# Kernel tuning notes

Hardware: AMD Instinct MI355X
Metric: run time of the kernel (lower is better)

The kernel has to match this reference:

```python
import jax, jax.numpy as jnp
import numpy as np

REG_DIAG = 0.01   # per-position regularizer added inside the loop in the original
REG_EPS = 1e-05   # global regularizer added after the loop


def setup_inputs() -> dict:
    key = jax.random.key(0)
    B, C, HW = 32, 128, 3136
    embedding = jax.random.normal(key, (B, C, HW), dtype=jnp.float32)
    return {"embedding": embedding}


def reference(embedding):
    # embedding: (B, C, HW)
    B, C, HW = embedding.shape
    mean = jnp.mean(embedding, axis=0)                     # (C, HW)
    centered = embedding - mean[None, :, :]                # (B, C, HW)
    # Per-position sample covariance: cov[i] = X_m^T X_m / (B-1), X_m = (B, C) slice at position i.
    cov = jnp.einsum('bci,bdi->icd', centered, centered) / (B - 1)  # (HW, C, C)
    eye = jnp.eye(C, dtype=embedding.dtype)
    cov = cov + (REG_DIAG + REG_EPS) * eye[None, :, :]
    inv_covariance = jnp.linalg.inv(cov)                   # batched inverse, (HW, C, C)
    return (mean, inv_covariance)
```

## Files before the change

### kernel.cpp

```cpp
#include <hip/hip_runtime.h>

#define HW 3136
#define NB 32
#define NC 128
#define XST 132
#define SST 36
#define LAMV 0.01001f
#define SIG(r) (((((r) & 1)) << 4) | ((r) >> 1))

static __device__ __forceinline__ float2 pka0(float2 c, float2 v, float2 a) {
  float2 d;
  asm("v_pk_fma_f32 %0, %1, %2, %3 op_sel:[0,0,0] op_sel_hi:[0,1,1]"
      : "=v"(d) : "v"(c), "v"(v), "v"(a));
  return d;
}
static __device__ __forceinline__ float2 pka1(float2 c, float2 v, float2 a) {
  float2 d;
  asm("v_pk_fma_f32 %0, %1, %2, %3 op_sel:[1,0,0] op_sel_hi:[1,1,1]"
      : "=v"(d) : "v"(c), "v"(v), "v"(a));
  return d;
}
static __device__ __forceinline__ float2 pke(float2 a, float2 b, float2 c) {
  float2 d;
  asm("v_pk_fma_f32 %0, %1, %2, %3"
      : "=v"(d) : "v"(a), "v"(b), "v"(c));
  return d;
}

__global__ __launch_bounds__(512, 8)
void mvg_kernel(const float* __restrict__ emb, float* __restrict__ out) {
  const int bid = blockIdx.x;
  const int pos = (bid & 7) * 392 + (bid >> 3);
  const int t = threadIdx.x;

  __shared__ __align__(16) float XcB[NB * XST];
  __shared__ __align__(16) float WB[NB * XST];
  __shared__ __align__(16) float SB[32 * SST];
  __shared__ __align__(16) float ms[NC];

  #pragma unroll
  for (int m = 0; m < 8; ++m) {
    const int idx = t + 512 * m;
    const int b = idx >> 7;
    const int c = idx & (NC - 1);
    XcB[SIG(b) * XST + c] = emb[(size_t)b * (size_t)(NC * HW) + (size_t)c * HW + pos];
  }
  __syncthreads();

  if (t < NC) {
    float s = 0.f;
    #pragma unroll
    for (int b = 0; b < NB; ++b) s += XcB[b * XST + t];
    const float m = s * (1.0f / NB);
    ms[t] = m;
    out[(size_t)t * HW + pos] = m;
  }
  __syncthreads();

  #pragma unroll
  for (int m = 0; m < 8; ++m) {
    const int idx = t + 512 * m;
    const int b = idx >> 7;
    const int c = idx & (NC - 1);
    XcB[b * XST + c] -= ms[c];
  }
  __syncthreads();

  if (t < 136) {
    const float fs = sqrtf(1089.0f - 8.0f * (float)t);
    const int I = (int)floorf((33.0f - fs) * 0.5f);
    const int J = I + t - (I * (33 - I)) / 2;
    const float* xi0 = &XcB[I * XST];
    const float* xi1 = &XcB[(16 + I) * XST];
    const float* xj0 = &XcB[J * XST];
    const float* xj1 = &XcB[(16 + J) * XST];
    float2 d00 = make_float2(0.f, 0.f), d01 = make_float2(0.f, 0.f);
    float2 d10 = make_float2(0.f, 0.f), d11 = make_float2(0.f, 0.f);
    #pragma unroll 8
    for (int c = 0; c < NC; c += 4) {
      const float4 a0 = *(const float4*)&xi0[c];
      const float4 a1 = *(const float4*)&xi1[c];
      const float4 b0 = *(const float4*)&xj0[c];
      const float4 b1 = *(const float4*)&xj1[c];
      const float2 a0L = make_float2(a0.x, a0.y), a0H = make_float2(a0.z, a0.w);
      const float2 a1L = make_float2(a1.x, a1.y), a1H = make_float2(a1.z, a1.w);
      const float2 b0L = make_float2(b0.x, b0.y), b0H = make_float2(b0.z, b0.w);
      const float2 b1L = make_float2(b1.x, b1.y), b1H = make_float2(b1.z, b1.w);
      d00 = pke(a0L, b0L, d00); d00 = pke(a0H, b0H, d00);
      d01 = pke(a0L, b1L, d01); d01 = pke(a0H, b1H, d01);
      d10 = pke(a1L, b0L, d10); d10 = pke(a1H, b0H, d10);
      d11 = pke(a1L, b1L, d11); d11 = pke(a1H, b1H, d11);
    }
    const float s31 = 1.0f / 31.0f;
    const float dg = (I == J) ? LAMV : 0.f;
    float2 e0, e1;
    e0.x = (d00.x + d00.y) * s31 + dg;
    e0.y = (d01.x + d01.y) * s31;
    e1.x = (d10.x + d10.y) * s31;
    e1.y = (d11.x + d11.y) * s31 + dg;
    *(float2*)&SB[I * SST + 2 * J] = e0;
    *(float2*)&SB[(16 + I) * SST + 2 * J] = e1;
    if (I != J) {
      *(float2*)&SB[J * SST + 2 * I] = make_float2(e0.x, e1.x);
      *(float2*)&SB[(16 + J) * SST + 2 * I] = make_float2(e0.y, e1.y);
    }
  }
  __syncthreads();

  if (t < 64) {
    const int r = t & 31;
    const int hb = (t >> 5) << 4;
    const int rs = SIG(r);
    float m[16];
    #pragma unroll
    for (int j = 0; j < 4; ++j) {
      const float4 v = *(const float4*)&SB[rs * SST + hb + 4 * j];
      m[4 * j] = v.x; m[4 * j + 1] = v.y; m[4 * j + 2] = v.z; m[4 * j + 3] = v.w;
    }

    #define SWEEP_K(K) {                                                    \
      float pc = m[(K) & 15] - ((r == (K)) ? 1.0f : 0.0f);                  \
      const float dm1 = __shfl(pc, (((K) >> 4) << 5) + (K), 64);            \
      const float cr  = __shfl(pc, (((K) >> 4) << 5) + r, 64);              \
      const float g = cr * __builtin_amdgcn_rcpf(dm1 + 1.0f);               \
      float hj[16];                                                         \
      _Pragma("unroll")                                                     \
      for (int j = 0; j < 16; ++j)                                          \
        hj[j] = __shfl(pc, (((K) >> 4) << 5) + hb + j, 64);                 \
      _Pragma("unroll")                                                     \
      for (int j = 0; j < 16; ++j) m[j] = fmaf(-g, hj[j], m[j]);            \
    }

    SWEEP_K(0)  SWEEP_K(1)  SWEEP_K(2)  SWEEP_K(3)
    SWEEP_K(4)  SWEEP_K(5)  SWEEP_K(6)  SWEEP_K(7)
    SWEEP_K(8)  SWEEP_K(9)  SWEEP_K(10) SWEEP_K(11)
    SWEEP_K(12) SWEEP_K(13) SWEEP_K(14) SWEEP_K(15)
    SWEEP_K(16) SWEEP_K(17) SWEEP_K(18) SWEEP_K(19)
    SWEEP_K(20) SWEEP_K(21) SWEEP_K(22) SWEEP_K(23)
    SWEEP_K(24) SWEEP_K(25) SWEEP_K(26) SWEEP_K(27)
    SWEEP_K(28) SWEEP_K(29) SWEEP_K(30) SWEEP_K(31)

    #pragma unroll
    for (int j = 0; j < 16; ++j) {
      const int col = hb + j;
      SB[rs * SST + col] = (col == r) ? (2.0f - m[j]) : (-m[j]);
    }
  }
  __syncthreads();

  if (t < 256) {
    const int s2 = t >> 4;
    const int CA = (t & 15) << 2;
    const int CB = 64 + CA;
    float2 w0[4], w1[4];
    #pragma unroll
    for (int q = 0; q < 4; ++q) {
      w0[q] = make_float2(0.f, 0.f);
      w1[q] = make_float2(0.f, 0.f);
    }
    #pragma unroll 2
    for (int j = 0; j < 32; j += 4) {
      const float4 sv0 = *(const float4*)&SB[s2 * SST + j];
      const float4 sv1 = *(const float4*)&SB[(16 + s2) * SST + j];
      const float2 s0L = make_float2(sv0.x, sv0.y), s0H = make_float2(sv0.z, sv0.w);
      const float2 s1L = make_float2(sv1.x, sv1.y), s1H = make_float2(sv1.z, sv1.w);
      const int jh = j >> 1;
      const float* xr0 = &XcB[jh * XST];
      const float* xr1 = &XcB[(16 + jh) * XST];
      const float* xr2 = &XcB[(jh + 1) * XST];
      const float* xr3 = &XcB[(17 + jh) * XST];
      {
        const float4 a = *(const float4*)&xr0[CA];
        const float4 b = *(const float4*)&xr0[CB];
        w0[0] = pka0(s0L, make_float2(a.x, a.y), w0[0]);
        w0[1] = pka0(s0L, make_float2(a.z, a.w), w0[1]);
        w0[2] = pka0(s0L, make_float2(b.x, b.y), w0[2]);
        w0[3] = pka0(s0L, make_float2(b.z, b.w), w0[3]);
        w1[0] = pka0(s1L, make_float2(a.x, a.y), w1[0]);
        w1[1] = pka0(s1L, make_float2(a.z, a.w), w1[1]);
        w1[2] = pka0(s1L, make_float2(b.x, b.y), w1[2]);
        w1[3] = pka0(s1L, make_float2(b.z, b.w), w1[3]);
      }
      {
        const float4 a = *(const float4*)&xr1[CA];
        const float4 b = *(const float4*)&xr1[CB];
        w0[0] = pka1(s0L, make_float2(a.x, a.y), w0[0]);
        w0[1] = pka1(s0L, make_float2(a.z, a.w), w0[1]);
        w0[2] = pka1(s0L, make_float2(b.x, b.y), w0[2]);
        w0[3] = pka1(s0L, make_float2(b.z, b.w), w0[3]);
        w1[0] = pka1(s1L, make_float2(a.x, a.y), w1[0]);
        w1[1] = pka1(s1L, make_float2(a.z, a.w), w1[1]);
        w1[2] = pka1(s1L, make_float2(b.x, b.y), w1[2]);
        w1[3] = pka1(s1L, make_float2(b.z, b.w), w1[3]);
      }
      {
        const float4 a = *(const float4*)&xr2[CA];
        const float4 b = *(const float4*)&xr2[CB];
        w0[0] = pka0(s0H, make_float2(a.x, a.y), w0[0]);
        w0[1] = pka0(s0H, make_float2(a.z, a.w), w0[1]);
        w0[2] = pka0(s0H, make_float2(b.x, b.y), w0[2]);
        w0[3] = pka0(s0H, make_float2(b.z, b.w), w0[3]);
        w1[0] = pka0(s1H, make_float2(a.x, a.y), w1[0]);
        w1[1] = pka0(s1H, make_float2(a.z, a.w), w1[1]);
        w1[2] = pka0(s1H, make_float2(b.x, b.y), w1[2]);
        w1[3] = pka0(s1H, make_float2(b.z, b.w), w1[3]);
      }
      {
        const float4 a = *(const float4*)&xr3[CA];
        const float4 b = *(const float4*)&xr3[CB];
        w0[0] = pka1(s0H, make_float2(a.x, a.y), w0[0]);
        w0[1] = pka1(s0H, make_float2(a.z, a.w), w0[1]);
        w0[2] = pka1(s0H, make_float2(b.x, b.y), w0[2]);
        w0[3] = pka1(s0H, make_float2(b.z, b.w), w0[3]);
        w1[0] = pka1(s1H, make_float2(a.x, a.y), w1[0]);
        w1[1] = pka1(s1H, make_float2(a.z, a.w), w1[1]);
        w1[2] = pka1(s1H, make_float2(b.x, b.y), w1[2]);
        w1[3] = pka1(s1H, make_float2(b.z, b.w), w1[3]);
      }
    }
    *(float4*)&WB[s2 * XST + CA] = make_float4(w0[0].x, w0[0].y, w0[1].x, w0[1].y);
    *(float4*)&WB[s2 * XST + CB] = make_float4(w0[2].x, w0[2].y, w0[3].x, w0[3].y);
    *(float4*)&WB[(16 + s2) * XST + CA] = make_float4(w1[0].x, w1[0].y, w1[1].x, w1[1].y);
    *(float4*)&WB[(16 + s2) * XST + CB] = make_float4(w1[2].x, w1[2].y, w1[3].x, w1[3].y);
  }
  __syncthreads();

  if (t < 272) {
    const int L = t >> 1;
    const int half = t & 1;
    const float fs = sqrtf(1089.0f - 8.0f * (float)L);
    const int R = (int)floorf((33.0f - fs) * 0.5f);
    const int C = R + L - (R * (33 - R)) / 2;
    const int r8 = R << 3;
    const int cb = (C << 3) + (half << 2);

    float2 aP[8][2];
    #pragma unroll
    for (int r = 0; r < 8; ++r) {
      aP[r][0] = make_float2(0.f, 0.f);
      aP[r][1] = make_float2(0.f, 0.f);
    }
    #pragma unroll 4
    for (int u = 0; u < 32; ++u) {
      const float4 cv0 = *(const float4*)&XcB[u * XST + r8];
      const float4 cv1 = *(const float4*)&XcB[u * XST + r8 + 4];
      const float4 rv  = *(const float4*)&WB[u * XST + cb];
      const float2 rL = make_float2(rv.x, rv.y), rH = make_float2(rv.z, rv.w);
      const float2 c01 = make_float2(cv0.x, cv0.y), c23 = make_float2(cv0.z, cv0.w);
      const float2 c45 = make_float2(cv1.x, cv1.y), c67 = make_float2(cv1.z, cv1.w);
      aP[0][0] = pka0(c01, rL, aP[0][0]); aP[0][1] = pka0(c01, rH, aP[0][1]);
      aP[1][0] = pka1(c01, rL, aP[1][0]); aP[1][1] = pka1(c01, rH, aP[1][1]);
      aP[2][0] = pka0(c23, rL, aP[2][0]); aP[2][1] = pka0(c23, rH, aP[2][1]);
      aP[3][0] = pka1(c23, rL, aP[3][0]); aP[3][1] = pka1(c23, rH, aP[3][1]);
      aP[4][0] = pka0(c45, rL, aP[4][0]); aP[4][1] = pka0(c45, rH, aP[4][1]);
      aP[5][0] = pka1(c45, rL, aP[5][0]); aP[5][1] = pka1(c45, rH, aP[5][1]);
      aP[6][0] = pka0(c67, rL, aP[6][0]); aP[6][1] = pka0(c67, rH, aP[6][1]);
      aP[7][0] = pka1(c67, rL, aP[7][0]); aP[7][1] = pka1(c67, rH, aP[7][1]);
    }

    const float ILAM = 1.0f / LAMV;
    const float IL31 = ILAM / 31.0f;
    float* o = out + (size_t)NC * HW + (size_t)pos * (NC * NC);

    #pragma unroll
    for (int r = 0; r < 8; ++r) {
      const int gr = r8 + r;
      float4 w;
      w.x = fmaf(-IL31, aP[r][0].x, (gr == cb + 0) ? ILAM : 0.f);
      w.y = fmaf(-IL31, aP[r][0].y, (gr == cb + 1) ? ILAM : 0.f);
      w.z = fmaf(-IL31, aP[r][1].x, (gr == cb + 2) ? ILAM : 0.f);
      w.w = fmaf(-IL31, aP[r][1].y, (gr == cb + 3) ? ILAM : 0.f);
      *(float4*)&o[(size_t)gr * NC + cb] = w;
    }

    if (R != C) {
      {
        const float4 m0 = make_float4(-IL31 * aP[0][0].x, -IL31 * aP[1][0].x,
                                      -IL31 * aP[2][0].x, -IL31 * aP[3][0].x);
        const float4 m1 = make_float4(-IL31 * aP[4][0].x, -IL31 * aP[5][0].x,
                                      -IL31 * aP[6][0].x, -IL31 * aP[7][0].x);
        *(float4*)&o[(size_t)(cb + 0) * NC + r8] = m0;
        *(float4*)&o[(size_t)(cb + 0) * NC + r8 + 4] = m1;
      }
      {
        const float4 m0 = make_float4(-IL31 * aP[0][0].y, -IL31 * aP[1][0].y,
                                      -IL31 * aP[2][0].y, -IL31 * aP[3][0].y);
        const float4 m1 = make_float4(-IL31 * aP[4][0].y, -IL31 * aP[5][0].y,
                                      -IL31 * aP[6][0].y, -IL31 * aP[7][0].y);
        *(float4*)&o[(size_t)(cb + 1) * NC + r8] = m0;
        *(float4*)&o[(size_t)(cb + 1) * NC + r8 + 4] = m1;
      }
      {
        const float4 m0 = make_float4(-IL31 * aP[0][1].x, -IL31 * aP[1][1].x,
                                      -IL31 * aP[2][1].x, -IL31 * aP[3][1].x);
        const float4 m1 = make_float4(-IL31 * aP[4][1].x, -IL31 * aP[5][1].x,
                                      -IL31 * aP[6][1].x, -IL31 * aP[7][1].x);
        *(float4*)&o[(size_t)(cb + 2) * NC + r8] = m0;
        *(float4*)&o[(size_t)(cb + 2) * NC + r8 + 4] = m1;
      }
      {
        const float4 m0 = make_float4(-IL31 * aP[0][1].y, -IL31 * aP[1][1].y,
                                      -IL31 * aP[2][1].y, -IL31 * aP[3][1].y);
        const float4 m1 = make_float4(-IL31 * aP[4][1].y, -IL31 * aP[5][1].y,
                                      -IL31 * aP[6][1].y, -IL31 * aP[7][1].y);
        *(float4*)&o[(size_t)(cb + 3) * NC + r8] = m0;
        *(float4*)&o[(size_t)(cb + 3) * NC + r8 + 4] = m1;
      }
    }
  }
}

extern "C" void kernel_launch(void* const* d_in, const int* in_sizes, int n_in,
                              void* d_out, int out_size, void* d_ws, size_t ws_size,
                              hipStream_t stream) {
  const float* emb = (const float*)d_in[0];
  float* out = (float*)d_out;
  mvg_kernel<<<HW, 512, 0, stream>>>(emb, out);
}
```

Before: 130.4 us.

## Split Gram reduction across thread pairs and retile S*X product stage

```diff
diff --git a/kernel.cpp b/kernel.cpp
--- a/kernel.cpp
+++ b/kernel.cpp
@@ -66,18 +66,22 @@
   }
   __syncthreads();
 
-  if (t < 136) {
-    const float fs = sqrtf(1089.0f - 8.0f * (float)t);
+  if (t < 272) {
+    const int L = t >> 1;
+    const int h = t & 1;
+    const float fs = sqrtf(1089.0f - 8.0f * (float)L);
     const int I = (int)floorf((33.0f - fs) * 0.5f);
-    const int J = I + t - (I * (33 - I)) / 2;
+    const int J = I + L - (I * (33 - I)) / 2;
     const float* xi0 = &XcB[I * XST];
     const float* xi1 = &XcB[(16 + I) * XST];
     const float* xj0 = &XcB[J * XST];
     const float* xj1 = &XcB[(16 + J) * XST];
+    const int cbase = h << 6;
     float2 d00 = make_float2(0.f, 0.f), d01 = make_float2(0.f, 0.f);
     float2 d10 = make_float2(0.f, 0.f), d11 = make_float2(0.f, 0.f);
     #pragma unroll 8
-    for (int c = 0; c < NC; c += 4) {
+    for (int cc = 0; cc < 64; cc += 4) {
+      const int c = cbase + cc;
       const float4 a0 = *(const float4*)&xi0[c];
       const float4 a1 = *(const float4*)&xi1[c];
       const float4 b0 = *(const float4*)&xj0[c];
@@ -91,18 +95,28 @@
       d10 = pke(a1L, b0L, d10); d10 = pke(a1H, b0H, d10);
       d11 = pke(a1L, b1L, d11); d11 = pke(a1H, b1H, d11);
     }
-    const float s31 = 1.0f / 31.0f;
-    const float dg = (I == J) ? LAMV : 0.f;
-    float2 e0, e1;
-    e0.x = (d00.x + d00.y) * s31 + dg;
-    e0.y = (d01.x + d01.y) * s31;
-    e1.x = (d10.x + d10.y) * s31;
-    e1.y = (d11.x + d11.y) * s31 + dg;
-    *(float2*)&SB[I * SST + 2 * J] = e0;
-    *(float2*)&SB[(16 + I) * SST + 2 * J] = e1;
-    if (I != J) {
-      *(float2*)&SB[J * SST + 2 * I] = make_float2(e0.x, e1.x);
-      *(float2*)&SB[(16 + J) * SST + 2 * I] = make_float2(e0.y, e1.y);
+    float s00 = d00.x + d00.y;
+    float s01 = d01.x + d01.y;
+    float s10 = d10.x + d10.y;
+    float s11 = d11.x + d11.y;
+    s00 += __shfl_xor(s00, 1);
+    s01 += __shfl_xor(s01, 1);
+    s10 += __shfl_xor(s10, 1);
+    s11 += __shfl_xor(s11, 1);
+    if (h == 0) {
+      const float s31 = 1.0f / 31.0f;
+      const float dg = (I == J) ? LAMV : 0.f;
+      float2 e0, e1;
+      e0.x = s00 * s31 + dg;
+      e0.y = s01 * s31;
+      e1.x = s10 * s31;
+      e1.y = s11 * s31 + dg;
+      *(float2*)&SB[I * SST + 2 * J] = e0;
+      *(float2*)&SB[(16 + I) * SST + 2 * J] = e1;
+      if (I != J) {
+        *(float2*)&SB[J * SST + 2 * I] = make_float2(e0.x, e1.x);
+        *(float2*)&SB[(16 + J) * SST + 2 * I] = make_float2(e0.y, e1.y);
+      }
     }
   }
   __syncthreads();
@@ -149,79 +163,51 @@
   __syncthreads();
 
   if (t < 256) {
-    const int s2 = t >> 4;
-    const int CA = (t & 15) << 2;
-    const int CB = 64 + CA;
-    float2 w0[4], w1[4];
-    #pragma unroll
-    for (int q = 0; q < 4; ++q) {
-      w0[q] = make_float2(0.f, 0.f);
-      w1[q] = make_float2(0.f, 0.f);
-    }
-    #pragma unroll 2
-    for (int j = 0; j < 32; j += 4) {
-      const float4 sv0 = *(const float4*)&SB[s2 * SST + j];
-      const float4 sv1 = *(const float4*)&SB[(16 + s2) * SST + j];
-      const float2 s0L = make_float2(sv0.x, sv0.y), s0H = make_float2(sv0.z, sv0.w);
-      const float2 s1L = make_float2(sv1.x, sv1.y), s1H = make_float2(sv1.z, sv1.w);
-      const int jh = j >> 1;
-      const float* xr0 = &XcB[jh * XST];
-      const float* xr1 = &XcB[(16 + jh) * XST];
-      const float* xr2 = &XcB[(jh + 1) * XST];
-      const float* xr3 = &XcB[(17 + jh) * XST];
-      {
-        const float4 a = *(const float4*)&xr0[CA];
-        const float4 b = *(const float4*)&xr0[CB];
-        w0[0] = pka0(s0L, make_float2(a.x, a.y), w0[0]);
-        w0[1] = pka0(s0L, make_float2(a.z, a.w), w0[1]);
-        w0[2] = pka0(s0L, make_float2(b.x, b.y), w0[2]);
-        w0[3] = pka0(s0L, make_float2(b.z, b.w), w0[3]);
-        w1[0] = pka0(s1L, make_float2(a.x, a.y), w1[0]);
-        w1[1] = pka0(s1L, make_float2(a.z, a.w), w1[1]);
-        w1[2] = pka0(s1L, make_float2(b.x, b.y), w1[2]);
-        w1[3] = pka0(s1L, make_float2(b.z, b.w), w1[3]);
-      }
-      {
-        const float4 a = *(const float4*)&xr1[CA];
-        const float4 b = *(const float4*)&xr1[CB];
-        w0[0] = pka1(s0L, make_float2(a.x, a.y), w0[0]);
-        w0[1] = pka1(s0L, make_float2(a.z, a.w), w0[1]);
-        w0[2] = pka1(s0L, make_float2(b.x, b.y), w0[2]);
-        w0[3] = pka1(s0L, make_float2(b.z, b.w), w0[3]);
-        w1[0] = pka1(s1L, make_float2(a.x, a.y), w1[0]);
-        w1[1] = pka1(s1L, make_float2(a.z, a.w), w1[1]);
-        w1[2] = pka1(s1L, make_float2(b.x, b.y), w1[2]);
-        w1[3] = pka1(s1L, make_float2(b.z, b.w), w1[3]);
-      }
-      {
-        const float4 a = *(const float4*)&xr2[CA];
-        const float4 b = *(const float4*)&xr2[CB];
-        w0[0] = pka0(s0H, make_float2(a.x, a.y), w0[0]);
-        w0[1] = pka0(s0H, make_float2(a.z, a.w), w0[1]);
-        w0[2] = pka0(s0H, make_float2(b.x, b.y), w0[2]);
-        w0[3] = pka0(s0H, make_float2(b.z, b.w), w0[3]);
-        w1[0] = pka0(s1H, make_float2(a.x, a.y), w1[0]);
-        w1[1] = pka0(s1H, make_float2(a.z, a.w), w1[1]);
-        w1[2] = pka0(s1H, make_float2(b.x, b.y), w1[2]);
-        w1[3] = pka0(s1H, make_float2(b.z, b.w), w1[3]);
-      }
-      {
-        const float4 a = *(const float4*)&xr3[CA];
-        const float4 b = *(const float4*)&xr3[CB];
-        w0[0] = pka1(s0H, make_float2(a.x, a.y), w0[0]);
-        w0[1] = pka1(s0H, make_float2(a.z, a.w), w0[1]);
-        w0[2] = pka1(s0H, make_float2(b.x, b.y), w0[2]);
-        w0[3] = pka1(s0H, make_float2(b.z, b.w), w0[3]);
-        w1[0] = pka1(s1H, make_float2(a.x, a.y), w1[0]);
-        w1[1] = pka1(s1H, make_float2(a.z, a.w), w1[1]);
-        w1[2] = pka1(s1H, make_float2(b.x, b.y), w1[2]);
-        w1[3] = pka1(s1H, make_float2(b.z, b.w), w1[3]);
-      }
-    }
-    *(float4*)&WB[s2 * XST + CA] = make_float4(w0[0].x, w0[0].y, w0[1].x, w0[1].y);
-    *(float4*)&WB[s2 * XST + CB] = make_float4(w0[2].x, w0[2].y, w0[3].x, w0[3].y);
-    *(float4*)&WB[(16 + s2) * XST + CA] = make_float4(w1[0].x, w1[0].y, w1[1].x, w1[1].y);
-    *(float4*)&WB[(16 + s2) * XST + CB] = make_float4(w1[2].x, w1[2].y, w1[3].x, w1[3].y);
+    const int g = t >> 5;
+    const int c0 = (t & 31) << 2;
+    const int sl0 = 2 * g, sl1 = 16 + 2 * g, sl2 = 2 * g + 1, sl3 = 17 + 2 * g;
+    float2 acc[4][2];
+    #pragma unroll
+    for (int r = 0; r < 4; ++r) {
+      acc[r][0] = make_float2(0.f, 0.f);
+      acc[r][1] = make_float2(0.f, 0.f);
+    }
+    #pragma unroll 4
+    for (int q = 0; q < 8; ++q) {
+      const float4 sv0 = *(const float4*)&SB[sl0 * SST + 4 * q];
+      const float4 sv1 = *(const float4*)&SB[sl1 * SST + 4 * q];
+      const float4 sv2 = *(const float4*)&SB[sl2 * SST + 4 * q];
+      const float4 sv3 = *(const float4*)&SB[sl3 * SST + 4 * q];
+      const float4 xv0 = *(const float4*)&XcB[(2 * q) * XST + c0];
+      const float4 xv1 = *(const float4*)&XcB[(16 + 2 * q) * XST + c0];
+      const float4 xv2 = *(const float4*)&XcB[(2 * q + 1) * XST + c0];
+      const float4 xv3 = *(const float4*)&XcB[(17 + 2 * q) * XST + c0];
+      const float2 x0L = make_float2(xv0.x, xv0.y), x0H = make_float2(xv0.z, xv0.w);
+      const float2 x1L = make_float2(xv1.x, xv1.y), x1H = make_float2(xv1.z, xv1.w);
+      const float2 x2L = make_float2(xv2.x, xv2.y), x2H = make_float2(xv2.z, xv2.w);
+      const float2 x3L = make_float2(xv3.x, xv3.y), x3H = make_float2(xv3.z, xv3.w);
+      #define P3ROW(R, SV) {                                              \
+        const float2 svL = make_float2(SV.x, SV.y);                       \
+        const float2 svH = make_float2(SV.z, SV.w);                       \
+        acc[R][0] = pka0(svL, x0L, acc[R][0]);                            \
+        acc[R][1] = pka0(svL, x0H, acc[R][1]);                            \
+        acc[R][0] = pka1(svL, x1L, acc[R][0]);                            \
+        acc[R][1] = pka1(svL, x1H, acc[R][1]);                            \
+        acc[R][0] = pka0(svH, x2L, acc[R][0]);                            \
+        acc[R][1] = pka0(svH, x2H, acc[R][1]);                            \
+        acc[R][0] = pka1(svH, x3L, acc[R][0]);                            \
+        acc[R][1] = pka1(svH, x3H, acc[R][1]);                            \
+      }
+      P3ROW(0, sv0)
+      P3ROW(1, sv1)
+      P3ROW(2, sv2)
+      P3ROW(3, sv3)
+      #undef P3ROW
+    }
+    *(float4*)&WB[sl0 * XST + c0] = make_float4(acc[0][0].x, acc[0][0].y, acc[0][1].x, acc[0][1].y);
+    *(float4*)&WB[sl1 * XST + c0] = make_float4(acc[1][0].x, acc[1][0].y, acc[1][1].x, acc[1][1].y);
+    *(float4*)&WB[sl2 * XST + c0] = make_float4(acc[2][0].x, acc[2][0].y, acc[2][1].x, acc[2][1].y);
+    *(float4*)&WB[sl3 * XST + c0] = make_float4(acc[3][0].x, acc[3][0].y, acc[3][1].x, acc[3][1].y);
   }
   __syncthreads();
 
```

Result: slower. 160.6 us (+23.1%).
